# Kernel tuning notes

Hardware: AMD Instinct MI355X
Metric: run time of the kernel (lower is better)

The kernel has to match this reference:

```python
import jax, jax.numpy as jnp
import numpy as np

NUM_HEADS = 8


def _mab(Q, K, Wq, bq, Wk, bk, Wv, bv, Wo, bo):
    # MAB with ln=False, dropout=0 (eval). Scale is sqrt(dim_V), matching source.
    B, Lq, _ = Q.shape
    Lk = K.shape[1]
    Dv = Wq.shape[1]
    dh = Dv // NUM_HEADS
    q = (Q @ Wq + bq).reshape(B, Lq, NUM_HEADS, dh).transpose(0, 2, 1, 3)
    k = (K @ Wk + bk).reshape(B, Lk, NUM_HEADS, dh).transpose(0, 2, 1, 3)
    v = (K @ Wv + bv).reshape(B, Lk, NUM_HEADS, dh).transpose(0, 2, 1, 3)
    A = jax.nn.softmax(jnp.einsum('bhqd,bhkd->bhqk', q, k) / jnp.sqrt(jnp.float32(Dv)), axis=-1)
    O = (q + jnp.einsum('bhqk,bhkd->bhqd', A, v)).transpose(0, 2, 1, 3).reshape(B, Lq, Dv)
    return O + jax.nn.relu(O @ Wo + bo)


def _forward(x, adj, gin_W, gin_b, geW1, geb1, geW2, geb2,
             gnW1, gnb1, gnW2, gnb2, goW, gob, S,
             mWq, mbq, mWk, mbk, mWv, mbv, mWo, mbo, finW, finb):
    B, V, T, D = x.shape
    Hd = gin_W.shape[1]
    # --- GNN encoder (adj path) ---
    h = x.reshape(B, V, T * D) @ gin_W + gin_b            # [B,V,H]
    # edge_mlp first linear on cat([h_i,h_j]) == h@Wi (row) + h@Wj (col); avoids 2H concat
    Wi, Wj = geW1[:Hd], geW1[Hd:]
    pre = (h @ Wi)[:, :, None, :] + (h @ Wj)[:, None, :, :] + geb1   # [B,V,V,H]
    e = jax.nn.relu(jax.nn.relu(pre) @ geW2 + geb2)       # [B,V,V,H]
    agg = jnp.einsum('bijh,bij->bih', e, adj)             # mask * sum over j, fused
    node = jax.nn.relu(jax.nn.relu(agg @ gnW1 + gnb1) @ gnW2 + gnb2)
    enc = node @ goW + gob                                # [B,V,H]
    # --- decoder: PMA + SAB + SAB + Linear ---
    o = _mab(jnp.broadcast_to(S, (B,) + S.shape[1:]), enc,
             mWq[0], mbq[0], mWk[0], mbk[0], mWv[0], mbv[0], mWo[0], mbo[0])
    o = _mab(o, o, mWq[1], mbq[1], mWk[1], mbk[1], mWv[1], mbv[1], mWo[1], mbo[1])
    o = _mab(o, o, mWq[2], mbq[2], mWk[2], mbk[2], mWv[2], mbv[2], mWo[2], mbo[2])
    out = o @ finW + finb                                 # [B,num_slots,T*OD]
    return out.reshape(B, S.shape[1], T, finW.shape[1] // T)


def setup_inputs() -> dict:
    key = jax.random.key(0)
    ks = jax.random.split(key, 16)
    B, V, T, D = 4, 256, 12, 4
    H, NS, OD = 256, 16, 32

    def w(k, shape, s=0.02):
        return s * jax.random.normal(k, shape, jnp.float32)

    return {
        'x': jax.random.normal(ks[0], (B, V, T, D), jnp.float32),
        'adj': (jax.random.uniform(ks[1], (B, V, V)) > 0.5).astype(jnp.float32),
        'gin_W': w(ks[2], (T * D, H)), 'gin_b': jnp.zeros((H,), jnp.float32),
        'geW1': w(ks[3], (2 * H, H)), 'geb1': jnp.zeros((H,), jnp.float32),
        'geW2': w(ks[4], (H, H)), 'geb2': jnp.zeros((H,), jnp.float32),
        'gnW1': w(ks[5], (H, H)), 'gnb1': jnp.zeros((H,), jnp.float32),
        'gnW2': w(ks[6], (H, H)), 'gnb2': jnp.zeros((H,), jnp.float32),
        'goW': w(ks[7], (H, H)), 'gob': jnp.zeros((H,), jnp.float32),
        'S': w(ks[8], (1, NS, H), 0.05),
        'mWq': w(ks[9], (3, H, H)), 'mbq': jnp.zeros((3, H), jnp.float32),
        'mWk': w(ks[10], (3, H, H)), 'mbk': jnp.zeros((3, H), jnp.float32),
        'mWv': w(ks[11], (3, H, H)), 'mbv': jnp.zeros((3, H), jnp.float32),
        'mWo': w(ks[12], (3, H, H)), 'mbo': jnp.zeros((3, H), jnp.float32),
        'finW': w(ks[13], (H, T * OD)), 'finb': jnp.zeros((T * OD,), jnp.float32),
    }


def reference(x, adj, gin_W, gin_b, geW1, geb1, geW2, geb2,
              gnW1, gnb1, gnW2, gnb2, goW, gob, S,
              mWq, mbq, mWk, mbk, mWv, mbv, mWo, mbo, finW, finb):
    return _forward(x, adj, gin_W, gin_b, geW1, geb1, geW2, geb2,
                    gnW1, gnb1, gnW2, gnb2, goW, gob, S,
                    mWq, mbq, mWk, mbk, mWv, mbv, mWo, mbo, finW, finb)
```

## Files before the change

kernel.cpp:

```cpp
#include <hip/hip_runtime.h>
#include <hip/hip_bf16.h>

typedef unsigned short u16;
typedef __bf16 bf8v __attribute__((ext_vector_type(8)));
typedef float f4v __attribute__((ext_vector_type(4)));

__device__ __forceinline__ float b2f(u16 v) {
  union { unsigned u; float f; } x; x.u = ((unsigned)v) << 16; return x.f;
}
__device__ __forceinline__ u16 f2b(float f) {
  union { float f; unsigned u; } x; x.f = f;
  unsigned r = (x.u + 0x7FFFu + ((x.u >> 16) & 1u)) >> 16;
  return (u16)r;
}
__device__ __forceinline__ unsigned pkbf(float a, float b) {
  union { __hip_bfloat162 h; unsigned u; } c;
  c.h = __float22bfloat162_rn(make_float2(a, b));
  return c.u;
}
__device__ __forceinline__ void up2(unsigned u, float& lo, float& hi) {
  union { unsigned x; float f; } a, b;
  a.x = u << 16; b.x = u & 0xffff0000u; lo = a.f; hi = b.f;
}

#define NFRAG 19
struct PreArgs {
  const float* fsrc[NFRAG];
  u16* fdst[NFRAG];
  int fstride[NFRAG];
  int fbase[NFRAG + 1];
  int fragTiles, hBase, prepBid, q1Bid;
  const float *x, *ginW, *ginb;
  u16* h_bf;
  const float *mbk, *mbv, *mbq, *S, *mWq;
  float *bkv0, *bqkv1, *bqkv2;
  u16* q1b;
};

__global__ __launch_bounds__(256) void k_pre(PreArgs a) {
  __shared__ u16 ld[256 * 20];
  __shared__ float xs[4][48];
  __shared__ float Ss[4096];
  const int bid = blockIdx.x, t = threadIdx.x;

  if (bid < a.fragTiles) {
    int j = 0;
    while (j + 1 < NFRAG && a.fbase[j + 1] <= bid) j++;
    const int localT = bid - a.fbase[j];
    const float* src = a.fsrc[j];
    const int Ns = a.fstride[j];
    const int n0 = localT * 16;
    {
      const float* s = src + (size_t)t * Ns + n0;
      const float4 v0 = ((const float4*)s)[0], v1 = ((const float4*)s)[1];
      const float4 v2 = ((const float4*)s)[2], v3 = ((const float4*)s)[3];
      unsigned* row = (unsigned*)(ld + t * 20);
      row[0] = pkbf(v0.x, v0.y); row[1] = pkbf(v0.z, v0.w);
      row[2] = pkbf(v1.x, v1.y); row[3] = pkbf(v1.z, v1.w);
      row[4] = pkbf(v2.x, v2.y); row[5] = pkbf(v2.z, v2.w);
      row[6] = pkbf(v3.x, v3.y); row[7] = pkbf(v3.z, v3.w);
    }
    __syncthreads();
    u16* dst = a.fdst[j] + (size_t)localT * 4096;
#pragma unroll
    for (int s2 = 0; s2 < 2; s2++) {
      const int o = t * 2 + s2, kt = o >> 6, lane = o & 63;
      const int nlo = lane & 15, bk = kt * 32 + ((lane >> 4) << 3);
      union { u16 h[8]; uint4 q; } pk;
#pragma unroll
      for (int j2 = 0; j2 < 8; j2++) pk.h[j2] = ld[(bk + j2) * 20 + nlo];
      *(uint4*)(dst + (size_t)(kt * 64 + lane) * 8) = pk.q;
    }
    return;
  }
  if (bid >= a.hBase && bid < a.hBase + 256) {
    const int row0 = (bid - a.hBase) * 4;
    if (t < 192) {
      const int rr = t / 48, k = t % 48;
      xs[rr][k] = a.x[(size_t)(row0 + rr) * 48 + k];
    }
    __syncthreads();
    const float bias = a.ginb[t];
    float acc[4] = {bias, bias, bias, bias};
    for (int k = 0; k < 48; k++) {
      const float w = a.ginW[(size_t)k * 256 + t];
#pragma unroll
      for (int rr = 0; rr < 4; rr++) acc[rr] += xs[rr][k] * w;
    }
#pragma unroll
    for (int rr = 0; rr < 4; rr++) a.h_bf[(size_t)(row0 + rr) * 256 + t] = f2b(acc[rr]);
    return;
  }
  if (bid == a.prepBid) {
    a.bkv0[t] = a.mbk[t]; a.bkv0[256 + t] = a.mbv[t];
    a.bqkv1[t] = a.mbq[256 + t]; a.bqkv1[256 + t] = a.mbk[256 + t]; a.bqkv1[512 + t] = a.mbv[256 + t];
    a.bqkv2[t] = a.mbq[512 + t]; a.bqkv2[256 + t] = a.mbk[512 + t]; a.bqkv2[512 + t] = a.mbv[512 + t];
    return;
  }
  if (bid == a.q1Bid) {
    for (int idx = t; idx < 4096; idx += 256) Ss[idx] = a.S[idx];
    __syncthreads();
    float acc[16];
#pragma unroll
    for (int r = 0; r < 16; r++) acc[r] = 0.f;
    for (int k = 0; k < 256; k++) {
      const float w = a.mWq[(size_t)k * 256 + t];
#pragma unroll
      for (int r = 0; r < 16; r++) acc[r] += Ss[r * 256 + k] * w;
    }
    const float bq = a.mbq[t];
#pragma unroll
    for (int r = 0; r < 16; r++) a.q1b[r * 256 + t] = f2b(acc[r] + bq);
    return;
  }
}

__global__ __launch_bounds__(256) void k_wiwj(
    const u16* __restrict__ h, const u16* __restrict__ frag,
    float* __restrict__ hWiF, u16* __restrict__ hWjB) {
  __shared__ __align__(16) u16 As[64 * 264];
  const int t = threadIdx.x, lane = t & 63, wv = t >> 6;
  const int m0 = blockIdx.x * 64, n0 = blockIdx.y * 128;
  {
    const int row = t >> 2, ch = t & 3;
#pragma unroll
    for (int s = 0; s < 8; s++)
      *(uint4*)(As + row * 264 + ch * 64 + s * 8) =
          *(const uint4*)(h + (size_t)(m0 + row) * 256 + ch * 64 + s * 8);
  }
  __syncthreads();
  f4v acc[4][2];
#pragma unroll
  for (int mt = 0; mt < 4; mt++)
#pragma unroll
    for (int nt = 0; nt < 2; nt++) acc[mt][nt] = (f4v){0.f, 0.f, 0.f, 0.f};
  const int Tw = (n0 >> 4) + wv * 2;
#pragma unroll
  for (int kt = 0; kt < 8; kt++) {
    bf8v af[4], bf[2];
#pragma unroll
    for (int mt = 0; mt < 4; mt++)
      af[mt] = *(const bf8v*)(As + (mt * 16 + (lane & 15)) * 264 + kt * 32 + ((lane >> 4) << 3));
#pragma unroll
    for (int nt = 0; nt < 2; nt++)
      bf[nt] = *(const bf8v*)(frag + ((size_t)((Tw + nt) * 8 + kt) * 64 + lane) * 8);
#pragma unroll
    for (int mt = 0; mt < 4; mt++)
#pragma unroll
      for (int nt = 0; nt < 2; nt++)
        acc[mt][nt] = __builtin_amdgcn_mfma_f32_16x16x32_bf16(af[mt], bf[nt], acc[mt][nt], 0, 0, 0);
  }
#pragma unroll
  for (int mt = 0; mt < 4; mt++)
#pragma unroll
    for (int nt = 0; nt < 2; nt++) {
      const int n = n0 + wv * 32 + nt * 16 + (lane & 15);
      const int mb = m0 + mt * 16 + ((lane >> 4) << 2);
#pragma unroll
      for (int r = 0; r < 4; r++) {
        if (n < 256)
          hWiF[(size_t)(mb + r) * 256 + n] = acc[mt][nt][r];
        else
          hWjB[(size_t)(mb + r) * 256 + (n - 256)] = f2b(acc[mt][nt][r]);
      }
    }
}

__global__ __launch_bounds__(256, 2) void k_edge(
    const float* __restrict__ hWiF, const u16* __restrict__ hWjB,
    const float* __restrict__ adj, const float* __restrict__ geb1,
    const u16* __restrict__ fragW2, const float* __restrict__ geb2,
    u16* __restrict__ aggB) {
  __shared__ __align__(16) u16 As[64 * 280];
  __shared__ float hi[256];
  __shared__ int jlist[256];
  __shared__ int cnt;
  const int t = threadIdx.x, lane = t & 63, wv = t >> 6;
  const int b = blockIdx.x >> 8, i = blockIdx.x & 255;
  if (t == 0) cnt = 0;
  __syncthreads();
  {
    const float a = adj[(size_t)(b * 256 + i) * 256 + t];
    hi[t] = hWiF[(size_t)(b * 256 + i) * 256 + t] + geb1[t];
    if (a != 0.f) { const int p = atomicAdd(&cnt, 1); jlist[p] = t; }
  }
  __syncthreads();
  const int nact = cnt;
  if (nact == 0) {
    if (lane < 16) {
#pragma unroll
      for (int nt = 0; nt < 4; nt++)
        aggB[(size_t)(b * 256 + i) * 256 + wv * 64 + nt * 16 + lane] = 0;
    }
    return;
  }
  const int nch = (nact + 63) >> 6;
  float bias2[4];
#pragma unroll
  for (int nt = 0; nt < 4; nt++) bias2[nt] = geb2[wv * 64 + nt * 16 + (lane & 15)];
  float aggAcc[4] = {0.f, 0.f, 0.f, 0.f};
  const u16* fw = fragW2 + lane * 8;

  for (int c = 0; c < nch; c++) {
    const int rows = min(64, nact - c * 64);
    {
      const int r = t >> 2, q = t & 3;
      const bool valid = (r < rows);
      const int j = valid ? jlist[c * 64 + r] : jlist[0];
      const uint4* s4 = (const uint4*)(hWjB + (size_t)(b * 256 + j) * 256 + q * 64);
      u16* dstrow = As + r * 280 + q * 72;
#pragma unroll
      for (int ii = 0; ii < 8; ii++) {
        const uint4 v = s4[ii];
        const int k = q * 64 + ii * 8;
        float f0, f1, f2, f3, f4, f5, f6, f7;
        up2(v.x, f0, f1); up2(v.y, f2, f3); up2(v.z, f4, f5); up2(v.w, f6, f7);
        uint4 qd;
        qd.x = pkbf(fmaxf(f0 + hi[k + 0], 0.f), fmaxf(f1 + hi[k + 1], 0.f));
        qd.y = pkbf(fmaxf(f2 + hi[k + 2], 0.f), fmaxf(f3 + hi[k + 3], 0.f));
        qd.z = pkbf(fmaxf(f4 + hi[k + 4], 0.f), fmaxf(f5 + hi[k + 5], 0.f));
        qd.w = pkbf(fmaxf(f6 + hi[k + 6], 0.f), fmaxf(f7 + hi[k + 7], 0.f));
        *(uint4*)(dstrow + ii * 8) = qd;
      }
    }
    __syncthreads();
    f4v acc[4][4];
#pragma unroll
    for (int jt = 0; jt < 4; jt++)
#pragma unroll
      for (int nt = 0; nt < 4; nt++) acc[jt][nt] = (f4v){0.f, 0.f, 0.f, 0.f};
    bf8v bcur[4];
#pragma unroll
    for (int nt = 0; nt < 4; nt++)
      bcur[nt] = *(const bf8v*)(fw + (size_t)((wv * 4 + nt) * 8 + 0) * 512);
#pragma unroll
    for (int kt = 0; kt < 8; kt++) {
      bf8v bnxt[4];
      if (kt < 7) {
#pragma unroll
        for (int nt = 0; nt < 4; nt++)
          bnxt[nt] = *(const bf8v*)(fw + (size_t)((wv * 4 + nt) * 8 + kt + 1) * 512);
      }
      bf8v af[4];
      const int coff = (kt >> 1) * 72 + (kt & 1) * 32 + ((lane >> 4) << 3);
#pragma unroll
      for (int jt = 0; jt < 4; jt++)
        af[jt] = *(const bf8v*)(As + (jt * 16 + (lane & 15)) * 280 + coff);
#pragma unroll
      for (int nt = 0; nt < 4; nt++)
#pragma unroll
        for (int jt = 0; jt < 4; jt++)
          acc[jt][nt] = __builtin_amdgcn_mfma_f32_16x16x32_bf16(af[jt], bcur[nt], acc[jt][nt], 0, 0, 0);
      if (kt < 7) {
#pragma unroll
        for (int nt = 0; nt < 4; nt++) bcur[nt] = bnxt[nt];
      }
    }
    const int rbase = (lane >> 4) * 4;
#pragma unroll
    for (int nt = 0; nt < 4; nt++) {
      float s = 0.f;
#pragma unroll
      for (int jt = 0; jt < 4; jt++) {
        const int r0 = jt * 16 + rbase;
#pragma unroll
        for (int r = 0; r < 4; r++) {
          const float e = fmaxf(acc[jt][nt][r] + bias2[nt], 0.f);
          s += (r0 + r < rows) ? e : 0.f;
        }
      }
      s += __shfl_xor(s, 16);
      s += __shfl_xor(s, 32);
      aggAcc[nt] += s;
    }
    __syncthreads();
  }
  if (lane < 16) {
#pragma unroll
    for (int nt = 0; nt < 4; nt++) {
      const int n = wv * 64 + nt * 16 + lane;
      aggB[(size_t)(b * 256 + i) * 256 + n] = f2b(aggAcc[nt]);
    }
  }
}

#define NBLK 32

__device__ __forceinline__ void gridbar(int* cnt, int gen) {
  __syncthreads();
  if (threadIdx.x == 0) {
    __threadfence();
    __hip_atomic_fetch_add(cnt, 1, __ATOMIC_RELAXED, __HIP_MEMORY_SCOPE_AGENT);
    int it = 0;
    while (__hip_atomic_load(cnt, __ATOMIC_RELAXED, __HIP_MEMORY_SCOPE_AGENT) < NBLK * gen) {
      __builtin_amdgcn_s_sleep(8);
      if (((++it) & 255) == 0)
        __hip_atomic_fetch_add(cnt, 0, __ATOMIC_RELAXED, __HIP_MEMORY_SCOPE_AGENT);
    }
    __threadfence();
  }
  __syncthreads();
}

__device__ void g32(const u16* Al, const u16* frag, const float* bias, int relu,
                    u16* Ol, int t) {
  const int lane = t & 63, wv = t >> 6;
  f4v acc[2][4];
#pragma unroll
  for (int mt = 0; mt < 2; mt++)
#pragma unroll
    for (int nt = 0; nt < 4; nt++) acc[mt][nt] = (f4v){0.f, 0.f, 0.f, 0.f};
#pragma unroll
  for (int kt = 0; kt < 8; kt++) {
    bf8v af[2], bf[4];
#pragma unroll
    for (int mt = 0; mt < 2; mt++)
      af[mt] = *(const bf8v*)(Al + (mt * 16 + (lane & 15)) * 264 + kt * 32 + ((lane >> 4) << 3));
#pragma unroll
    for (int nt = 0; nt < 4; nt++)
      bf[nt] = *(const bf8v*)(frag + ((size_t)((wv * 4 + nt) * 8 + kt) * 64 + lane) * 8);
#pragma unroll
    for (int mt = 0; mt < 2; mt++)
#pragma unroll
      for (int nt = 0; nt < 4; nt++)
        acc[mt][nt] = __builtin_amdgcn_mfma_f32_16x16x32_bf16(af[mt], bf[nt], acc[mt][nt], 0, 0, 0);
  }
#pragma unroll
  for (int mt = 0; mt < 2; mt++)
#pragma unroll
    for (int nt = 0; nt < 4; nt++) {
      const int col = wv * 64 + nt * 16 + (lane & 15);
      const float bv = bias[col];
#pragma unroll
      for (int r = 0; r < 4; r++) {
        const int row = mt * 16 + ((lane >> 4) << 2) + r;
        float v = acc[mt][nt][r] + bv;
        if (relu) v = fmaxf(v, 0.f);
        Ol[row * 264 + col] = f2b(v);
      }
    }
}

__device__ void g32kv(const u16* Al, const u16* frag, const float* bias,
                      u16* outG, int t) {
  const int lane = t & 63, wv = t >> 6;
  f4v acc[2][8];
#pragma unroll
  for (int mt = 0; mt < 2; mt++)
#pragma unroll
    for (int nt = 0; nt < 8; nt++) acc[mt][nt] = (f4v){0.f, 0.f, 0.f, 0.f};
#pragma unroll
  for (int kt = 0; kt < 8; kt++) {
    bf8v af[2];
#pragma unroll
    for (int mt = 0; mt < 2; mt++)
      af[mt] = *(const bf8v*)(Al + (mt * 16 + (lane & 15)) * 264 + kt * 32 + ((lane >> 4) << 3));
#pragma unroll
    for (int nt = 0; nt < 8; nt++) {
      const bf8v bf = *(const bf8v*)(frag + ((size_t)((wv * 8 + nt) * 8 + kt) * 64 + lane) * 8);
#pragma unroll
      for (int mt = 0; mt < 2; mt++)
        acc[mt][nt] = __builtin_amdgcn_mfma_f32_16x16x32_bf16(af[mt], bf, acc[mt][nt], 0, 0, 0);
    }
  }
#pragma unroll
  for (int mt = 0; mt < 2; mt++)
#pragma unroll
    for (int nt = 0; nt < 8; nt++) {
      const int col = wv * 128 + nt * 16 + (lane & 15);
      const float bv = bias[col];
#pragma unroll
      for (int r = 0; r < 4; r++) {
        const int row = mt * 16 + ((lane >> 4) << 2) + r;
        outG[(size_t)row * 512 + col] = f2b(acc[mt][nt][r] + bv);
      }
    }
}

__device__ void attn_tile(const u16* __restrict__ qbuf,
                          const u16* __restrict__ kbuf, const u16* __restrict__ vbuf,
                          float* __restrict__ oF, u16* __restrict__ oB,
                          int b, int hd, float* qs, float* sc, float* vs, int t) {
  const int lane = t & 63, wv = t >> 6;
  const int Lk = 256;
  if (t < 64) {
    const int row = t >> 2, part = t & 3;
    const uint4 q4 = *(const uint4*)(qbuf + (size_t)row * 256 + hd * 32 + part * 8);
    float f0, f1, f2, f3, f4, f5, f6, f7;
    up2(q4.x, f0, f1); up2(q4.y, f2, f3); up2(q4.z, f4, f5); up2(q4.w, f6, f7);
    float4* d = (float4*)(qs + row * 32 + part * 8);
    d[0] = make_float4(f0, f1, f2, f3);
    d[1] = make_float4(f4, f5, f6, f7);
  }
  __syncthreads();
  {
    float kv[32];
    const uint4* kp = (const uint4*)(kbuf + (size_t)(b * Lk + t) * 512 + hd * 32);
#pragma unroll
    for (int c4 = 0; c4 < 4; c4++) {
      const uint4 k4 = kp[c4];
      up2(k4.x, kv[c4 * 8 + 0], kv[c4 * 8 + 1]);
      up2(k4.y, kv[c4 * 8 + 2], kv[c4 * 8 + 3]);
      up2(k4.z, kv[c4 * 8 + 4], kv[c4 * 8 + 5]);
      up2(k4.w, kv[c4 * 8 + 6], kv[c4 * 8 + 7]);
    }
    for (int r = 0; r < 16; r++) {
      float s = 0.f;
#pragma unroll
      for (int d = 0; d < 32; d++) s += qs[r * 32 + d] * kv[d];
      sc[r * 256 + t] = s * 0.0625f;
    }
  }
  __syncthreads();
  for (int r = wv * 4; r < wv * 4 + 4; r++) {
    float v[4];
    float mx = -1e30f;
#pragma unroll
    for (int q2 = 0; q2 < 4; q2++) {
      v[q2] = sc[r * 256 + lane + q2 * 64];
      mx = fmaxf(mx, v[q2]);
    }
    for (int off = 32; off; off >>= 1) mx = fmaxf(mx, __shfl_xor(mx, off));
    float sum = 0.f;
#pragma unroll
    for (int q2 = 0; q2 < 4; q2++) { v[q2] = __expf(v[q2] - mx); sum += v[q2]; }
    for (int off = 32; off; off >>= 1) sum += __shfl_xor(sum, off);
    const float inv = 1.f / sum;
#pragma unroll
    for (int q2 = 0; q2 < 4; q2++) sc[r * 256 + lane + q2 * 64] = v[q2] * inv;
  }
  __syncthreads();
  for (int u = t; u < 1024; u += 256) {
    const int row = u >> 2, part = u & 3;
    const uint4 v4 = *(const uint4*)(vbuf + (size_t)(b * Lk + row) * 512 + hd * 32 + part * 8);
    float f0, f1, f2, f3, f4, f5, f6, f7;
    up2(v4.x, f0, f1); up2(v4.y, f2, f3); up2(v4.z, f4, f5); up2(v4.w, f6, f7);
    float4* d = (float4*)(vs + row * 32 + part * 8);
    d[0] = make_float4(f0, f1, f2, f3);
    d[1] = make_float4(f4, f5, f6, f7);
  }
  __syncthreads();
  const int r0 = t >> 5, d = t & 31;
  float a0 = qs[r0 * 32 + d], a1 = qs[(r0 + 8) * 32 + d];
#pragma unroll 4
  for (int j = 0; j < Lk; j++) {
    const float vv = vs[j * 32 + d];
    a0 += sc[r0 * 256 + j] * vv;
    a1 += sc[(r0 + 8) * 256 + j] * vv;
  }
  const int c0 = hd * 32 + d;
  oF[(size_t)(b * 16 + r0) * 256 + c0] = a0;
  oB[(size_t)(b * 16 + r0) * 256 + c0] = f2b(a0);
  oF[(size_t)(b * 16 + r0 + 8) * 256 + c0] = a1;
  oB[(size_t)(b * 16 + r0 + 8) * 256 + c0] = f2b(a1);
}

__device__ void wprojG(const u16* __restrict__ o1b, const float* __restrict__ o1f,
                       const u16* __restrict__ frag, const float* __restrict__ bias,
                       u16* actL, float* residL, int b, int T, int lane) {
  f4v acc = (f4v){0.f, 0.f, 0.f, 0.f};
  const u16* abase = o1b + (size_t)(b * 16 + (lane & 15)) * 256 + ((lane >> 4) << 3);
  const u16* fbase = frag + ((size_t)(T * 8) * 64 + lane) * 8;
#pragma unroll
  for (int kt = 0; kt < 8; kt++)
    acc = __builtin_amdgcn_mfma_f32_16x16x32_bf16(*(const bf8v*)(abase + kt * 32),
                                                  *(const bf8v*)(fbase + (size_t)kt * 512), acc, 0, 0, 0);
  const int col = T * 16 + (lane & 15);
  const float bv = bias[col];
#pragma unroll
  for (int r = 0; r < 4; r++) {
    const int row = ((lane >> 4) << 2) + r;
    const float v = fmaxf(acc[r] + bv, 0.f) + o1f[(size_t)(b * 16 + row) * 256 + col];
    residL[row * 256 + col] = v;
    actL[row * 264 + col] = f2b(v);
  }
}

__device__ void wprojQ(const u16* actL, const u16* __restrict__ frag,
                       const float* __restrict__ bias, u16* qkvL, int T, int lane) {
  f4v acc = (f4v){0.f, 0.f, 0.f, 0.f};
  const u16* abase = actL + (lane & 15) * 264 + ((lane >> 4) << 3);
  const u16* fbase = frag + ((size_t)(T * 8) * 64 + lane) * 8;
#pragma unroll
  for (int kt = 0; kt < 8; kt++)
    acc = __builtin_amdgcn_mfma_f32_16x16x32_bf16(*(const bf8v*)(abase + kt * 32),
                                                  *(const bf8v*)(fbase + (size_t)kt * 512), acc, 0, 0, 0);
  const int col = T * 16 + (lane & 15);
  const float bv = bias[col];
#pragma unroll
  for (int r = 0; r < 4; r++) {
    const int row = ((lane >> 4) << 2) + r;
    qkvL[row * 776 + col] = f2b(acc[r] + bv);
  }
}

__device__ void wprojR(const u16* actIn, const u16* __restrict__ frag,
                       const float* __restrict__ bias, u16* actOut, float* residL,
                       int T, int lane) {
  f4v acc = (f4v){0.f, 0.f, 0.f, 0.f};
  const u16* abase = actIn + (lane & 15) * 264 + ((lane >> 4) << 3);
  const u16* fbase = frag + ((size_t)(T * 8) * 64 + lane) * 8;
#pragma unroll
  for (int kt = 0; kt < 8; kt++)
    acc = __builtin_amdgcn_mfma_f32_16x16x32_bf16(*(const bf8v*)(abase + kt * 32),
                                                  *(const bf8v*)(fbase + (size_t)kt * 512), acc, 0, 0, 0);
  const int col = T * 16 + (lane & 15);
  const float bv = bias[col];
#pragma unroll
  for (int r = 0; r < 4; r++) {
    const int row = ((lane >> 4) << 2) + r;
    const float v = fmaxf(acc[r] + bv, 0.f) + residL[row * 256 + col];
    residL[row * 256 + col] = v;
    actOut[row * 264 + col] = f2b(v);
  }
}

__device__ void wprojF(const u16* actL, const u16* __restrict__ frag,
                       const float* __restrict__ bias, float* __restrict__ outG,
                       int T, int lane) {
  f4v acc = (f4v){0.f, 0.f, 0.f, 0.f};
  const u16* abase = actL + (lane & 15) * 264 + ((lane >> 4) << 3);
  const u16* fbase = frag + ((size_t)(T * 8) * 64 + lane) * 8;
#pragma unroll
  for (int kt = 0; kt < 8; kt++)
    acc = __builtin_amdgcn_mfma_f32_16x16x32_bf16(*(const bf8v*)(abase + kt * 32),
                                                  *(const bf8v*)(fbase + (size_t)kt * 512), acc, 0, 0, 0);
  const int col = T * 16 + (lane & 15);
  const float bv = bias[col];
#pragma unroll
  for (int r = 0; r < 4; r++) {
    const int row = ((lane >> 4) << 2) + r;
    outG[(size_t)row * 384 + col] = acc[r] + bv;
  }
}

__device__ void attnB(const u16* qkvL, float* residL, u16* actOut, float* ps,
                      int hd, int lane) {
  const int r = lane & 15, cg = lane >> 4;
  float qv[32];
  {
    const uint4* qp = (const uint4*)(qkvL + r * 776 + hd * 32);
#pragma unroll
    for (int c4 = 0; c4 < 4; c4++) {
      const uint4 q4 = qp[c4];
      up2(q4.x, qv[c4 * 8 + 0], qv[c4 * 8 + 1]);
      up2(q4.y, qv[c4 * 8 + 2], qv[c4 * 8 + 3]);
      up2(q4.z, qv[c4 * 8 + 4], qv[c4 * 8 + 5]);
      up2(q4.w, qv[c4 * 8 + 6], qv[c4 * 8 + 7]);
    }
  }
  float p[4];
#pragma unroll
  for (int c = 0; c < 4; c++) {
    const int cc = cg * 4 + c;
    const uint4* kp = (const uint4*)(qkvL + cc * 776 + 256 + hd * 32);
    float s = 0.f;
#pragma unroll
    for (int c4 = 0; c4 < 4; c4++) {
      const uint4 k4 = kp[c4];
      float k0, k1;
      up2(k4.x, k0, k1); s += qv[c4 * 8 + 0] * k0 + qv[c4 * 8 + 1] * k1;
      up2(k4.y, k0, k1); s += qv[c4 * 8 + 2] * k0 + qv[c4 * 8 + 3] * k1;
      up2(k4.z, k0, k1); s += qv[c4 * 8 + 4] * k0 + qv[c4 * 8 + 5] * k1;
      up2(k4.w, k0, k1); s += qv[c4 * 8 + 6] * k0 + qv[c4 * 8 + 7] * k1;
    }
    p[c] = s * 0.0625f;
  }
  float mx = fmaxf(fmaxf(p[0], p[1]), fmaxf(p[2], p[3]));
  mx = fmaxf(mx, __shfl_xor(mx, 16));
  mx = fmaxf(mx, __shfl_xor(mx, 32));
  float sum = 0.f;
#pragma unroll
  for (int c = 0; c < 4; c++) { p[c] = __expf(p[c] - mx); sum += p[c]; }
  sum += __shfl_xor(sum, 16);
  sum += __shfl_xor(sum, 32);
  const float inv = 1.f / sum;
#pragma unroll
  for (int c = 0; c < 4; c++) ps[r * 16 + cg * 4 + c] = p[c] * inv;
  float o[8];
#pragma unroll
  for (int j = 0; j < 8; j++) o[j] = qv[cg * 8 + j];
#pragma unroll
  for (int c = 0; c < 16; c++) {
    const float pv = ps[r * 16 + c];
    const uint4 v4 = *(const uint4*)(qkvL + c * 776 + 512 + hd * 32 + cg * 8);
    float v0, v1;
    up2(v4.x, v0, v1); o[0] += pv * v0; o[1] += pv * v1;
    up2(v4.y, v0, v1); o[2] += pv * v0; o[3] += pv * v1;
    up2(v4.z, v0, v1); o[4] += pv * v0; o[5] += pv * v1;
    up2(v4.w, v0, v1); o[6] += pv * v0; o[7] += pv * v1;
  }
  const int col0 = hd * 32 + cg * 8;
#pragma unroll
  for (int j = 0; j < 8; j++) residL[r * 256 + col0 + j] = o[j];
  unsigned* ob = (unsigned*)(actOut + r * 264 + col0);
  ob[0] = pkbf(o[0], o[1]); ob[1] = pkbf(o[2], o[3]);
  ob[2] = pkbf(o[4], o[5]); ob[3] = pkbf(o[6], o[7]);
}

struct TailArgs {
  const u16 *agg, *fGn1, *fGn2, *fGo, *fKV0, *fQKV1, *fQKV2, *fO0, *fO1, *fO2, *fFin, *q1b;
  const float *gnb1, *gnb2, *gob, *bkv0, *bqkv1, *bqkv2, *mbo, *finb;
  u16 *kv1, *o1b;
  float *o1f, *outF;
  int* bar;
};

__global__ __launch_bounds__(256) void k_tail(TailArgs a) {
  __shared__ __align__(16) char smem[62208];
  const int bid = blockIdx.x, t = threadIdx.x;
  const int lane = t & 63, w = t >> 6;

  {
    u16* actA = (u16*)smem;
    u16* actB = (u16*)(smem + 16896);
    const int r0 = bid * 32;
#pragma unroll
    for (int s = 0; s < 4; s++) {
      const int u = t * 4 + s, row = u >> 5, ch = u & 31;
      *(uint4*)(actA + row * 264 + ch * 8) =
          *(const uint4*)(a.agg + (size_t)(r0 + row) * 256 + ch * 8);
    }
    __syncthreads();
    g32(actA, a.fGn1, a.gnb1, 1, actB, t); __syncthreads();
    g32(actB, a.fGn2, a.gnb2, 1, actA, t); __syncthreads();
    g32(actA, a.fGo, a.gob, 0, actB, t); __syncthreads();
    g32kv(actB, a.fKV0, a.bkv0, a.kv1 + (size_t)r0 * 512, t);
  }
  gridbar(a.bar, 1);
  {
    float* qs = (float*)smem;
    float* sc = (float*)(smem + 2048);
    float* vs = (float*)(smem + 18432);
    attn_tile(a.q1b, a.kv1, a.kv1 + 256, a.o1f, a.o1b, bid >> 3, bid & 7, qs, sc, vs, t);
  }
  gridbar(a.bar, 2);
  if (bid >= 4) return;
  {
    const int b = bid;
    u16* act0 = (u16*)smem;
    u16* act1 = (u16*)(smem + 8448);
    u16* qkvL = (u16*)(smem + 16896);
    float* residL = (float*)(smem + 41728);
    float* psL = (float*)(smem + 58112);
    __syncthreads();
    for (int T = w; T < 16; T += 4) wprojG(a.o1b, a.o1f, a.fO0, a.mbo, act0, residL, b, T, lane);
    __syncthreads();
    for (int T = w; T < 48; T += 4) wprojQ(act0, a.fQKV1, a.bqkv1, qkvL, T, lane);
    __syncthreads();
    for (int hd = w; hd < 8; hd += 4) attnB(qkvL, residL, act1, psL + w * 256, hd, lane);
    __syncthreads();
    for (int T = w; T < 16; T += 4) wprojR(act1, a.fO1, a.mbo + 256, act0, residL, T, lane);
    __syncthreads();
    for (int T = w; T < 48; T += 4) wprojQ(act0, a.fQKV2, a.bqkv2, qkvL, T, lane);
    __syncthreads();
    for (int hd = w; hd < 8; hd += 4) attnB(qkvL, residL, act1, psL + w * 256, hd, lane);
    __syncthreads();
    for (int T = w; T < 16; T += 4) wprojR(act1, a.fO2, a.mbo + 512, act0, residL, T, lane);
    __syncthreads();
    for (int T = w; T < 24; T += 4)
      wprojF(act0, a.fFin, a.finb, a.outF + (size_t)b * 16 * 384, T, lane);
  }
}

extern "C" void kernel_launch(void* const* d_in, const int* in_sizes, int n_in,
                              void* d_out, int out_size, void* d_ws, size_t ws_size,
                              hipStream_t stream) {
  const float* x    = (const float*)d_in[0];
  const float* adj  = (const float*)d_in[1];
  const float* ginW = (const float*)d_in[2];
  const float* ginb = (const float*)d_in[3];
  const float* geW1 = (const float*)d_in[4];
  const float* geb1 = (const float*)d_in[5];
  const float* geW2 = (const float*)d_in[6];
  const float* geb2 = (const float*)d_in[7];
  const float* gnW1 = (const float*)d_in[8];
  const float* gnb1 = (const float*)d_in[9];
  const float* gnW2 = (const float*)d_in[10];
  const float* gnb2 = (const float*)d_in[11];
  const float* goW  = (const float*)d_in[12];
  const float* gob  = (const float*)d_in[13];
  const float* S    = (const float*)d_in[14];
  const float* mWq  = (const float*)d_in[15];
  const float* mbq  = (const float*)d_in[16];
  const float* mWk  = (const float*)d_in[17];
  const float* mbk  = (const float*)d_in[18];
  const float* mWv  = (const float*)d_in[19];
  const float* mbv  = (const float*)d_in[20];
  const float* mWo  = (const float*)d_in[21];
  const float* mbo  = (const float*)d_in[22];
  const float* finW = (const float*)d_in[23];
  const float* finb = (const float*)d_in[24];
  (void)in_sizes; (void)n_in; (void)out_size; (void)ws_size;

  char* wp = (char*)d_ws;
  size_t off = 0;
  auto alloc = [&](size_t bytes) -> char* {
    char* p = wp + off;
    off += (bytes + 255) & ~(size_t)255;
    return p;
  };
  u16* h_bf     = (u16*)alloc(1024 * 256 * 2);
  float* hWiF   = (float*)alloc((size_t)1024 * 256 * 4);
  u16* hWjB     = (u16*)alloc(1024 * 256 * 2);
  u16* fWiWj    = (u16*)alloc(512 * 256 * 2);
  u16* fW2      = (u16*)alloc(256 * 256 * 2);
  u16* fGn1     = (u16*)alloc(256 * 256 * 2);
  u16* fGn2     = (u16*)alloc(256 * 256 * 2);
  u16* fGo      = (u16*)alloc(256 * 256 * 2);
  u16* fQ0      = (u16*)alloc(256 * 256 * 2);
  u16* fKV0     = (u16*)alloc(512 * 256 * 2);
  u16* fQKV1    = (u16*)alloc(768 * 256 * 2);
  u16* fQKV2    = (u16*)alloc(768 * 256 * 2);
  u16* fO0      = (u16*)alloc(256 * 256 * 2);
  u16* fO1      = (u16*)alloc(256 * 256 * 2);
  u16* fO2      = (u16*)alloc(256 * 256 * 2);
  u16* fFin     = (u16*)alloc(384 * 256 * 2);
  float* bkv0   = (float*)alloc(512 * 4);
  float* bqkv1  = (float*)alloc(768 * 4);
  float* bqkv2  = (float*)alloc(768 * 4);
  u16* q1b      = (u16*)alloc(16 * 256 * 2);
  u16* agg_b    = (u16*)alloc(1024 * 256 * 2);
  u16* kv1      = (u16*)alloc(1024 * 512 * 2);
  float* o1f    = (float*)alloc(64 * 256 * 4);
  u16* o1b      = (u16*)alloc(64 * 256 * 2);
  int* bar      = (int*)alloc(256);

  PreArgs P{};
  int nj = 0, tiles = 0;
  auto addF = [&](const float* s, int stride, u16* d, int nT) {
    P.fsrc[nj] = s; P.fdst[nj] = d; P.fstride[nj] = stride; P.fbase[nj] = tiles;
    tiles += nT; nj++;
  };
  addF(geW1, 256, fWiWj, 16);
  addF(geW1 + 65536, 256, fWiWj + 16 * 4096, 16);
  addF(geW2, 256, fW2, 16);
  addF(gnW1, 256, fGn1, 16);
  addF(gnW2, 256, fGn2, 16);
  addF(goW, 256, fGo, 16);
  addF(mWq, 256, fQ0, 16);
  addF(mWk, 256, fKV0, 16);
  addF(mWv, 256, fKV0 + 16 * 4096, 16);
  addF(mWq + 65536, 256, fQKV1, 16);
  addF(mWk + 65536, 256, fQKV1 + 16 * 4096, 16);
  addF(mWv + 65536, 256, fQKV1 + 32 * 4096, 16);
  addF(mWq + 131072, 256, fQKV2, 16);
  addF(mWk + 131072, 256, fQKV2 + 16 * 4096, 16);
  addF(mWv + 131072, 256, fQKV2 + 32 * 4096, 16);
  addF(mWo, 256, fO0, 16);
  addF(mWo + 65536, 256, fO1, 16);
  addF(mWo + 131072, 256, fO2, 16);
  addF(finW, 384, fFin, 24);
  P.fbase[nj] = tiles;
  P.fragTiles = tiles;
  P.hBase = tiles;
  P.prepBid = tiles + 256;
  P.q1Bid = tiles + 257;
  P.x = x; P.ginW = ginW; P.ginb = ginb; P.h_bf = h_bf;
  P.mbk = mbk; P.mbv = mbv; P.mbq = mbq; P.S = S; P.mWq = mWq;
  P.bkv0 = bkv0; P.bqkv1 = bqkv1; P.bqkv2 = bqkv2; P.q1b = q1b;

  TailArgs T{};
  T.agg = agg_b; T.fGn1 = fGn1; T.fGn2 = fGn2; T.fGo = fGo; T.fKV0 = fKV0;
  T.fQKV1 = fQKV1; T.fQKV2 = fQKV2; T.fO0 = fO0; T.fO1 = fO1; T.fO2 = fO2;
  T.fFin = fFin; T.q1b = q1b;
  T.gnb1 = gnb1; T.gnb2 = gnb2; T.gob = gob;
  T.bkv0 = bkv0; T.bqkv1 = bqkv1; T.bqkv2 = bqkv2; T.mbo = mbo; T.finb = finb;
  T.kv1 = kv1; T.o1b = o1b; T.o1f = o1f; T.outF = (float*)d_out;
  T.bar = bar;

  hipMemsetAsync(bar, 0, 256, stream);
  k_pre<<<dim3(tiles + 258), dim3(256), 0, stream>>>(P);
  k_wiwj<<<dim3(16, 4), dim3(256), 0, stream>>>(h_bf, fWiWj, hWiF, hWjB);
  k_edge<<<dim3(1024), dim3(256), 0, stream>>>(hWiF, hWjB, adj, geb1, fW2, geb2, agg_b);
  k_tail<<<dim3(NBLK), dim3(256), 0, stream>>>(T);
}
```

Baseline: 243.5 us.

## Split persistent tail kernel into three launches and prefetch next edge chunk

Replaces the single 32-block tail kernel, which used software grid barriers, with three separate kernel launches: node MLP plus KV projection, PMA attention, and the SAB decoder, which now runs with 512 threads per block. This removes the spin-wait grid barriers and their memset in exchange for two extra launch overheads. In the edge kernel, the hWjB rows for the next 64-row chunk are loaded into registers while the current chunk runs its MFMAs, hiding global load latency at the cost of extra registers. The decoder stage now uses 8 waves, one attention head per wave.

```diff
diff --git a/kernel.cpp b/kernel.cpp
--- a/kernel.cpp
+++ b/kernel.cpp
@@ -200,18 +200,24 @@
   for (int nt = 0; nt < 4; nt++) bias2[nt] = geb2[wv * 64 + nt * 16 + (lane & 15)];
   float aggAcc[4] = {0.f, 0.f, 0.f, 0.f};
   const u16* fw = fragW2 + lane * 8;
+  const int r = t >> 2, q = t & 3;
+
+  uint4 G[8];
+  {
+    const int rows0 = min(64, nact);
+    const int j = (r < rows0) ? jlist[r] : jlist[0];
+    const uint4* s4 = (const uint4*)(hWjB + (size_t)(b * 256 + j) * 256 + q * 64);
+#pragma unroll
+    for (int ii = 0; ii < 8; ii++) G[ii] = s4[ii];
+  }
 
   for (int c = 0; c < nch; c++) {
     const int rows = min(64, nact - c * 64);
     {
-      const int r = t >> 2, q = t & 3;
-      const bool valid = (r < rows);
-      const int j = valid ? jlist[c * 64 + r] : jlist[0];
-      const uint4* s4 = (const uint4*)(hWjB + (size_t)(b * 256 + j) * 256 + q * 64);
       u16* dstrow = As + r * 280 + q * 72;
 #pragma unroll
       for (int ii = 0; ii < 8; ii++) {
-        const uint4 v = s4[ii];
+        const uint4 v = G[ii];
         const int k = q * 64 + ii * 8;
         float f0, f1, f2, f3, f4, f5, f6, f7;
         up2(v.x, f0, f1); up2(v.y, f2, f3); up2(v.z, f4, f5); up2(v.w, f6, f7);
@@ -224,6 +230,13 @@
       }
     }
     __syncthreads();
+    if (c + 1 < nch) {
+      const int rowsN = min(64, nact - (c + 1) * 64);
+      const int j = (r < rowsN) ? jlist[(c + 1) * 64 + r] : jlist[0];
+      const uint4* s4 = (const uint4*)(hWjB + (size_t)(b * 256 + j) * 256 + q * 64);
+#pragma unroll
+      for (int ii = 0; ii < 8; ii++) G[ii] = s4[ii];
+    }
     f4v acc[4][4];
 #pragma unroll
     for (int jt = 0; jt < 4; jt++)
@@ -264,9 +277,9 @@
       for (int jt = 0; jt < 4; jt++) {
         const int r0 = jt * 16 + rbase;
 #pragma unroll
-        for (int r = 0; r < 4; r++) {
-          const float e = fmaxf(acc[jt][nt][r] + bias2[nt], 0.f);
-          s += (r0 + r < rows) ? e : 0.f;
+        for (int rr = 0; rr < 4; rr++) {
+          const float e = fmaxf(acc[jt][nt][rr] + bias2[nt], 0.f);
+          s += (r0 + rr < rows) ? e : 0.f;
         }
       }
       s += __shfl_xor(s, 16);
@@ -282,24 +295,6 @@
       aggB[(size_t)(b * 256 + i) * 256 + n] = f2b(aggAcc[nt]);
     }
   }
-}
-
-#define NBLK 32
-
-__device__ __forceinline__ void gridbar(int* cnt, int gen) {
-  __syncthreads();
-  if (threadIdx.x == 0) {
-    __threadfence();
-    __hip_atomic_fetch_add(cnt, 1, __ATOMIC_RELAXED, __HIP_MEMORY_SCOPE_AGENT);
-    int it = 0;
-    while (__hip_atomic_load(cnt, __ATOMIC_RELAXED, __HIP_MEMORY_SCOPE_AGENT) < NBLK * gen) {
-      __builtin_amdgcn_s_sleep(8);
-      if (((++it) & 255) == 0)
-        __hip_atomic_fetch_add(cnt, 0, __ATOMIC_RELAXED, __HIP_MEMORY_SCOPE_AGENT);
-    }
-    __threadfence();
-  }
-  __syncthreads();
 }
 
 __device__ void g32(const u16* Al, const u16* frag, const float* bias, int relu,
@@ -377,15 +372,44 @@
     }
 }
 
-__device__ void attn_tile(const u16* __restrict__ qbuf,
-                          const u16* __restrict__ kbuf, const u16* __restrict__ vbuf,
-                          float* __restrict__ oF, u16* __restrict__ oB,
-                          int b, int hd, float* qs, float* sc, float* vs, int t) {
+struct TailArgs {
+  const u16 *agg, *fGn1, *fGn2, *fGo, *fKV0, *fQKV1, *fQKV2, *fO0, *fO1, *fO2, *fFin, *q1b;
+  const float *gnb1, *gnb2, *gob, *bkv0, *bqkv1, *bqkv2, *mbo, *finb;
+  u16 *kv1, *o1b;
+  float *o1f, *outF;
+};
+
+__global__ __launch_bounds__(256) void k_tail1(TailArgs a) {
+  __shared__ __align__(16) char smem[33792];
+  const int bid = blockIdx.x, t = threadIdx.x;
+  u16* actA = (u16*)smem;
+  u16* actB = (u16*)(smem + 16896);
+  const int r0 = bid * 32;
+#pragma unroll
+  for (int s = 0; s < 4; s++) {
+    const int u = t * 4 + s, row = u >> 5, ch = u & 31;
+    *(uint4*)(actA + row * 264 + ch * 8) =
+        *(const uint4*)(a.agg + (size_t)(r0 + row) * 256 + ch * 8);
+  }
+  __syncthreads();
+  g32(actA, a.fGn1, a.gnb1, 1, actB, t); __syncthreads();
+  g32(actB, a.fGn2, a.gnb2, 1, actA, t); __syncthreads();
+  g32(actA, a.fGo, a.gob, 0, actB, t); __syncthreads();
+  g32kv(actB, a.fKV0, a.bkv0, a.kv1 + (size_t)r0 * 512, t);
+}
+
+__global__ __launch_bounds__(256) void k_tail2(TailArgs a) {
+  __shared__ __align__(16) char smem[51200];
+  const int bid = blockIdx.x, t = threadIdx.x;
   const int lane = t & 63, wv = t >> 6;
+  const int b = bid >> 3, hd = bid & 7;
+  float* qs = (float*)smem;
+  float* sc = (float*)(smem + 2048);
+  float* vs = (float*)(smem + 18432);
   const int Lk = 256;
   if (t < 64) {
     const int row = t >> 2, part = t & 3;
-    const uint4 q4 = *(const uint4*)(qbuf + (size_t)row * 256 + hd * 32 + part * 8);
+    const uint4 q4 = *(const uint4*)(a.q1b + (size_t)row * 256 + hd * 32 + part * 8);
     float f0, f1, f2, f3, f4, f5, f6, f7;
     up2(q4.x, f0, f1); up2(q4.y, f2, f3); up2(q4.z, f4, f5); up2(q4.w, f6, f7);
     float4* d = (float4*)(qs + row * 32 + part * 8);
@@ -395,7 +419,7 @@
   __syncthreads();
   {
     float kv[32];
-    const uint4* kp = (const uint4*)(kbuf + (size_t)(b * Lk + t) * 512 + hd * 32);
+    const uint4* kp = (const uint4*)(a.kv1 + (size_t)(b * Lk + t) * 512 + hd * 32);
 #pragma unroll
     for (int c4 = 0; c4 < 4; c4++) {
       const uint4 k4 = kp[c4];
@@ -432,7 +456,7 @@
   __syncthreads();
   for (int u = t; u < 1024; u += 256) {
     const int row = u >> 2, part = u & 3;
-    const uint4 v4 = *(const uint4*)(vbuf + (size_t)(b * Lk + row) * 512 + hd * 32 + part * 8);
+    const uint4 v4 = *(const uint4*)(a.kv1 + (size_t)(b * Lk + row) * 512 + 256 + hd * 32 + part * 8);
     float f0, f1, f2, f3, f4, f5, f6, f7;
     up2(v4.x, f0, f1); up2(v4.y, f2, f3); up2(v4.z, f4, f5); up2(v4.w, f6, f7);
     float4* d = (float4*)(vs + row * 32 + part * 8);
@@ -449,10 +473,10 @@
     a1 += sc[(r0 + 8) * 256 + j] * vv;
   }
   const int c0 = hd * 32 + d;
-  oF[(size_t)(b * 16 + r0) * 256 + c0] = a0;
-  oB[(size_t)(b * 16 + r0) * 256 + c0] = f2b(a0);
-  oF[(size_t)(b * 16 + r0 + 8) * 256 + c0] = a1;
-  oB[(size_t)(b * 16 + r0 + 8) * 256 + c0] = f2b(a1);
+  a.o1f[(size_t)(b * 16 + r0) * 256 + c0] = a0;
+  a.o1b[(size_t)(b * 16 + r0) * 256 + c0] = f2b(a0);
+  a.o1f[(size_t)(b * 16 + r0 + 8) * 256 + c0] = a1;
+  a.o1b[(size_t)(b * 16 + r0 + 8) * 256 + c0] = f2b(a1);
 }
 
 __device__ void wprojG(const u16* __restrict__ o1b, const float* __restrict__ o1f,
@@ -598,69 +622,32 @@
   ob[2] = pkbf(o[4], o[5]); ob[3] = pkbf(o[6], o[7]);
 }
 
-struct TailArgs {
-  const u16 *agg, *fGn1, *fGn2, *fGo, *fKV0, *fQKV1, *fQKV2, *fO0, *fO1, *fO2, *fFin, *q1b;
-  const float *gnb1, *gnb2, *gob, *bkv0, *bqkv1, *bqkv2, *mbo, *finb;
-  u16 *kv1, *o1b;
-  float *o1f, *outF;
-  int* bar;
-};
-
-__global__ __launch_bounds__(256) void k_tail(TailArgs a) {
-  __shared__ __align__(16) char smem[62208];
-  const int bid = blockIdx.x, t = threadIdx.x;
+__global__ __launch_bounds__(512) void k_tail3(TailArgs a) {
+  __shared__ __align__(16) char smem[66304];
+  const int b = blockIdx.x, t = threadIdx.x;
   const int lane = t & 63, w = t >> 6;
-
-  {
-    u16* actA = (u16*)smem;
-    u16* actB = (u16*)(smem + 16896);
-    const int r0 = bid * 32;
-#pragma unroll
-    for (int s = 0; s < 4; s++) {
-      const int u = t * 4 + s, row = u >> 5, ch = u & 31;
-      *(uint4*)(actA + row * 264 + ch * 8) =
-          *(const uint4*)(a.agg + (size_t)(r0 + row) * 256 + ch * 8);
-    }
-    __syncthreads();
-    g32(actA, a.fGn1, a.gnb1, 1, actB, t); __syncthreads();
-    g32(actB, a.fGn2, a.gnb2, 1, actA, t); __syncthreads();
-    g32(actA, a.fGo, a.gob, 0, actB, t); __syncthreads();
-    g32kv(actB, a.fKV0, a.bkv0, a.kv1 + (size_t)r0 * 512, t);
-  }
-  gridbar(a.bar, 1);
-  {
-    float* qs = (float*)smem;
-    float* sc = (float*)(smem + 2048);
-    float* vs = (float*)(smem + 18432);
-    attn_tile(a.q1b, a.kv1, a.kv1 + 256, a.o1f, a.o1b, bid >> 3, bid & 7, qs, sc, vs, t);
-  }
-  gridbar(a.bar, 2);
-  if (bid >= 4) return;
-  {
-    const int b = bid;
-    u16* act0 = (u16*)smem;
-    u16* act1 = (u16*)(smem + 8448);
-    u16* qkvL = (u16*)(smem + 16896);
-    float* residL = (float*)(smem + 41728);
-    float* psL = (float*)(smem + 58112);
-    __syncthreads();
-    for (int T = w; T < 16; T += 4) wprojG(a.o1b, a.o1f, a.fO0, a.mbo, act0, residL, b, T, lane);
-    __syncthreads();
-    for (int T = w; T < 48; T += 4) wprojQ(act0, a.fQKV1, a.bqkv1, qkvL, T, lane);
-    __syncthreads();
-    for (int hd = w; hd < 8; hd += 4) attnB(qkvL, residL, act1, psL + w * 256, hd, lane);
-    __syncthreads();
-    for (int T = w; T < 16; T += 4) wprojR(act1, a.fO1, a.mbo + 256, act0, residL, T, lane);
-    __syncthreads();
-    for (int T = w; T < 48; T += 4) wprojQ(act0, a.fQKV2, a.bqkv2, qkvL, T, lane);
-    __syncthreads();
-    for (int hd = w; hd < 8; hd += 4) attnB(qkvL, residL, act1, psL + w * 256, hd, lane);
-    __syncthreads();
-    for (int T = w; T < 16; T += 4) wprojR(act1, a.fO2, a.mbo + 512, act0, residL, T, lane);
-    __syncthreads();
-    for (int T = w; T < 24; T += 4)
-      wprojF(act0, a.fFin, a.finb, a.outF + (size_t)b * 16 * 384, T, lane);
-  }
+  u16* act0 = (u16*)smem;
+  u16* act1 = (u16*)(smem + 8448);
+  u16* qkvL = (u16*)(smem + 16896);
+  float* residL = (float*)(smem + 41728);
+  float* psL = (float*)(smem + 58112);
+
+  for (int T = w; T < 16; T += 8) wprojG(a.o1b, a.o1f, a.fO0, a.mbo, act0, residL, b, T, lane);
+  __syncthreads();
+  for (int T = w; T < 48; T += 8) wprojQ(act0, a.fQKV1, a.bqkv1, qkvL, T, lane);
+  __syncthreads();
+  if (w < 8) attnB(qkvL, residL, act1, psL + w * 256, w, lane);
+  __syncthreads();
+  for (int T = w; T < 16; T += 8) wprojR(act1, a.fO1, a.mbo + 256, act0, residL, T, lane);
+  __syncthreads();
+  for (int T = w; T < 48; T += 8) wprojQ(act0, a.fQKV2, a.bqkv2, qkvL, T, lane);
+  __syncthreads();
+  if (w < 8) attnB(qkvL, residL, act1, psL + w * 256, w, lane);
+  __syncthreads();
+  for (int T = w; T < 16; T += 8) wprojR(act1, a.fO2, a.mbo + 512, act0, residL, T, lane);
+  __syncthreads();
+  for (int T = w; T < 24; T += 8)
+    wprojF(act0, a.fFin, a.finb, a.outF + (size_t)b * 16 * 384, T, lane);
 }
 
 extern "C" void kernel_launch(void* const* d_in, const int* in_sizes, int n_in,
@@ -724,7 +711,6 @@
   u16* kv1      = (u16*)alloc(1024 * 512 * 2);
   float* o1f    = (float*)alloc(64 * 256 * 4);
   u16* o1b      = (u16*)alloc(64 * 256 * 2);
-  int* bar      = (int*)alloc(256);
 
   PreArgs P{};
   int nj = 0, tiles = 0;
@@ -767,11 +753,11 @@
   T.gnb1 = gnb1; T.gnb2 = gnb2; T.gob = gob;
   T.bkv0 = bkv0; T.bqkv1 = bqkv1; T.bqkv2 = bqkv2; T.mbo = mbo; T.finb = finb;
   T.kv1 = kv1; T.o1b = o1b; T.o1f = o1f; T.outF = (float*)d_out;
-  T.bar = bar;
-
-  hipMemsetAsync(bar, 0, 256, stream);
+
   k_pre<<<dim3(tiles + 258), dim3(256), 0, stream>>>(P);
   k_wiwj<<<dim3(16, 4), dim3(256), 0, stream>>>(h_bf, fWiWj, hWiF, hWjB);
   k_edge<<<dim3(1024), dim3(256), 0, stream>>>(hWiF, hWjB, adj, geb1, fW2, geb2, agg_b);
-  k_tail<<<dim3(NBLK), dim3(256), 0, stream>>>(T);
-}
+  k_tail1<<<dim3(32), dim3(256), 0, stream>>>(T);
+  k_tail2<<<dim3(32), dim3(256), 0, stream>>>(T);
+  k_tail3<<<dim3(4), dim3(512), 0, stream>>>(T);
+}
```

After: 251.8 us. 1.03x slower.
